# Kernel tuning notes

Measured on AMD Instinct MI355X. Metric: run time of the kernel, lower is better.

## Reference

```python
import jax, jax.numpy as jnp
import numpy as np

SHAPE = (160, 192, 224)  # target warp volume shape (D, H, W)
SHIFT_CENTER = True
BATCH = 4


def setup_inputs() -> dict:
    key = jax.random.key(0)
    # small random affine perturbation around identity-ish values
    matrix = jax.random.normal(key, (BATCH, 3, 4), dtype=jnp.float32)
    return {"matrix": matrix}


def _mesh(shape, shift_center, dtype):
    # ij-indexed coordinate grid, stacked last: [D, H, W, 3]
    grids = jnp.meshgrid(*[jnp.arange(d, dtype=dtype) for d in shape], indexing="ij")
    mesh = jnp.stack(grids, axis=-1)
    if shift_center:
        center = (jnp.asarray(shape, dtype=dtype) - 1) / 2
        mesh = mesh - center
    return mesh


def reference(matrix) -> jnp.ndarray:
    """Affine [B,3,4] -> dense shift [B, D, H, W, 3].

    Equivalent to: loc = A @ [mesh; 1]; return loc - mesh, per batch element.
    """
    dtype = matrix.dtype
    mesh = _mesh(SHAPE, SHIFT_CENTER, dtype)  # [D,H,W,3]
    A = matrix[:, :, :3]                      # [B,3,3] linear part
    t = matrix[:, :, 3]                       # [B,3]   translation
    # affine-transformed coordinates minus original coordinates
    loc = jnp.einsum("bij,dhwj->bdhwi", A, mesh) + t[:, None, None, None, :]
    return loc - mesh[None]
```

## Files before the change

### kernel.cpp

```cpp
#include <hip/hip_runtime.h>

#define D_DIM 160
#define H_DIM 192
#define W_DIM 224
#define BLOCK 256
#define F4PT 6

__global__ __launch_bounds__(BLOCK) void AffineToDenseShift_kernel(
    const float* __restrict__ matrix, float* __restrict__ out) {
  const int b = blockIdx.y;
  const float* M = matrix + b * 12;

  const float a00 = M[0] - 1.0f, a01 = M[1],        a02 = M[2],         t0 = M[3];
  const float a10 = M[4],        a11 = M[5] - 1.0f, a12 = M[6],         t1 = M[7];
  const float a20 = M[8],        a21 = M[9],        a22 = M[10] - 1.0f, t2 = M[11];

  const long long batch_floats = (long long)D_DIM * H_DIM * W_DIM * 3;
  float4* __restrict__ dst = (float4*)(out + (long long)b * batch_floats);

  const unsigned fbase = blockIdx.x * (BLOCK * F4PT) + threadIdx.x;

  #pragma unroll
  for (int k = 0; k < F4PT; ++k) {
    const unsigned f = fbase + (unsigned)k * BLOCK;
    const unsigned L = 4u * f;
    const unsigned v = L / 3u;
    const unsigned p = L - 3u * v;

    const unsigned w = v % (unsigned)W_DIM;
    const unsigned r = v / (unsigned)W_DIM;
    const unsigned h = r % (unsigned)H_DIM;
    const unsigned d = r / (unsigned)H_DIM;

    const float md = (float)d - (float)(D_DIM - 1) * 0.5f;
    const float mh = (float)h - (float)(H_DIM - 1) * 0.5f;
    const float mw = (float)w - (float)(W_DIM - 1) * 0.5f;

    const float x0 = fmaf(a00, md, fmaf(a01, mh, fmaf(a02, mw, t0)));
    const float y0 = fmaf(a10, md, fmaf(a11, mh, fmaf(a12, mw, t1)));
    const float z0 = fmaf(a20, md, fmaf(a21, mh, fmaf(a22, mw, t2)));

    const bool ww = (w == (unsigned)(W_DIM - 1));
    const bool hw = ww && (h == (unsigned)(H_DIM - 1));
    const float mw1 = ww ? -(float)(W_DIM - 1) * 0.5f : mw + 1.0f;
    const float mh1 = hw ? -(float)(H_DIM - 1) * 0.5f : (ww ? mh + 1.0f : mh);
    const float md1 = hw ? md + 1.0f : md;

    const float x1 = fmaf(a00, md1, fmaf(a01, mh1, fmaf(a02, mw1, t0)));
    const float y1 = fmaf(a10, md1, fmaf(a11, mh1, fmaf(a12, mw1, t1)));
    const float z1 = fmaf(a20, md1, fmaf(a21, mh1, fmaf(a22, mw1, t2)));

    float4 o;
    o.x = (p == 0u) ? x0 : ((p == 1u) ? y0 : z0);
    o.y = (p == 0u) ? y0 : ((p == 1u) ? z0 : x1);
    o.z = (p == 0u) ? z0 : ((p == 1u) ? x1 : y1);
    o.w = (p == 0u) ? x1 : ((p == 1u) ? y1 : z1);
    dst[f] = o;
  }
}

extern "C" void kernel_launch(void* const* d_in, const int* in_sizes, int n_in,
                              void* d_out, int out_size, void* d_ws, size_t ws_size,
                              hipStream_t stream) {
  const float* matrix = (const float*)d_in[0];
  float* out = (float*)d_out;

  const int batch = in_sizes[0] / 12;
  const long long batch_f4 = (long long)D_DIM * H_DIM * W_DIM * 3 / 4;
  const int blocks_x = (int)((batch_f4 + (long long)BLOCK * F4PT - 1) /
                             ((long long)BLOCK * F4PT));

  dim3 grid(blocks_x, batch);
  AffineToDenseShift_kernel<<<grid, BLOCK, 0, stream>>>(matrix, out);
}
```

Before: 61.63 us.

## Compute four voxels per thread and stage through LDS for coalesced stores

Each thread now computes four consecutive voxels, deriving three of them with incremental adds of the W-column coefficients, which relies on W being a multiple of 4. The interleaved xyz results are written to shared memory and then copied out as fully coalesced float4 stores. This removes the per-element divide/modulo and select logic of the old per-float4 mapping. In exchange it adds LDS traffic and two block barriers per iteration, and the repeated adds may differ slightly from the direct FMA in rounding.

```diff
diff --git a/kernel.cpp b/kernel.cpp
--- a/kernel.cpp
+++ b/kernel.cpp
@@ -4,10 +4,12 @@
 #define H_DIM 192
 #define W_DIM 224
 #define BLOCK 256
-#define F4PT 6
+#define S_ITERS 2
 
 __global__ __launch_bounds__(BLOCK) void AffineToDenseShift_kernel(
     const float* __restrict__ matrix, float* __restrict__ out) {
+  __shared__ alignas(16) float lds[3 * 1024];
+
   const int b = blockIdx.y;
   const float* M = matrix + b * 12;
 
@@ -16,16 +18,17 @@
   const float a20 = M[8],        a21 = M[9],        a22 = M[10] - 1.0f, t2 = M[11];
 
   const long long batch_floats = (long long)D_DIM * H_DIM * W_DIM * 3;
-  float4* __restrict__ dst = (float4*)(out + (long long)b * batch_floats);
+  float4* __restrict__ dst4 = (float4*)(out + (long long)b * batch_floats);
 
-  const unsigned fbase = blockIdx.x * (BLOCK * F4PT) + threadIdx.x;
+  const unsigned t = threadIdx.x;
+  const unsigned vbase0 = blockIdx.x * (1024u * S_ITERS) + 4u * t;
+  const unsigned f4base0 = blockIdx.x * (768u * S_ITERS) + t;
+
+  float4* const Lw = (float4*)&lds[12u * t];
 
   #pragma unroll
-  for (int k = 0; k < F4PT; ++k) {
-    const unsigned f = fbase + (unsigned)k * BLOCK;
-    const unsigned L = 4u * f;
-    const unsigned v = L / 3u;
-    const unsigned p = L - 3u * v;
+  for (int s = 0; s < S_ITERS; ++s) {
+    const unsigned v = vbase0 + (unsigned)s * 1024u;
 
     const unsigned w = v % (unsigned)W_DIM;
     const unsigned r = v / (unsigned)W_DIM;
@@ -39,23 +42,21 @@
     const float x0 = fmaf(a00, md, fmaf(a01, mh, fmaf(a02, mw, t0)));
     const float y0 = fmaf(a10, md, fmaf(a11, mh, fmaf(a12, mw, t1)));
     const float z0 = fmaf(a20, md, fmaf(a21, mh, fmaf(a22, mw, t2)));
+    const float x1 = x0 + a02, y1 = y0 + a12, z1 = z0 + a22;
+    const float x2 = x1 + a02, y2 = y1 + a12, z2 = z1 + a22;
+    const float x3 = x2 + a02, y3 = y2 + a12, z3 = z2 + a22;
 
-    const bool ww = (w == (unsigned)(W_DIM - 1));
-    const bool hw = ww && (h == (unsigned)(H_DIM - 1));
-    const float mw1 = ww ? -(float)(W_DIM - 1) * 0.5f : mw + 1.0f;
-    const float mh1 = hw ? -(float)(H_DIM - 1) * 0.5f : (ww ? mh + 1.0f : mh);
-    const float md1 = hw ? md + 1.0f : md;
+    Lw[0] = make_float4(x0, y0, z0, x1);
+    Lw[1] = make_float4(y1, z1, x2, y2);
+    Lw[2] = make_float4(z2, x3, y3, z3);
+    __syncthreads();
 
-    const float x1 = fmaf(a00, md1, fmaf(a01, mh1, fmaf(a02, mw1, t0)));
-    const float y1 = fmaf(a10, md1, fmaf(a11, mh1, fmaf(a12, mw1, t1)));
-    const float z1 = fmaf(a20, md1, fmaf(a21, mh1, fmaf(a22, mw1, t2)));
-
-    float4 o;
-    o.x = (p == 0u) ? x0 : ((p == 1u) ? y0 : z0);
-    o.y = (p == 0u) ? y0 : ((p == 1u) ? z0 : x1);
-    o.z = (p == 0u) ? z0 : ((p == 1u) ? x1 : y1);
-    o.w = (p == 0u) ? x1 : ((p == 1u) ? y1 : z1);
-    dst[f] = o;
+    const float4* const Ls = (const float4*)lds;
+    float4* const dc = dst4 + (f4base0 + (unsigned)s * 768u - t);
+    dc[t]        = Ls[t];
+    dc[t + 256u] = Ls[t + 256u];
+    dc[t + 512u] = Ls[t + 512u];
+    __syncthreads();
   }
 }
 
@@ -66,9 +67,8 @@
   float* out = (float*)d_out;
 
   const int batch = in_sizes[0] / 12;
-  const long long batch_f4 = (long long)D_DIM * H_DIM * W_DIM * 3 / 4;
-  const int blocks_x = (int)((batch_f4 + (long long)BLOCK * F4PT - 1) /
-                             ((long long)BLOCK * F4PT));
+  const long long per_batch_vox = (long long)D_DIM * H_DIM * W_DIM;
+  const int blocks_x = (int)(per_batch_vox / (1024LL * S_ITERS));
 
   dim3 grid(blocks_x, batch);
   AffineToDenseShift_kernel<<<grid, BLOCK, 0, stream>>>(matrix, out);
```

Result: faster. 59.51 us (-3.5%).
